# Kernel optimization log

Measured on AMD Instinct MI355X. Metric: run time of the kernel, lower is better.

The kernel has to match this reference:

```python
import jax, jax.numpy as jnp
import numpy as np

H = 51  # hidden size hard-coded in the module

def _lstm_cell(x_t, h, c, W_ih, W_hh, b_ih, b_hh):
    # PyTorch LSTMCell gate order: i, f, g, o
    gates = x_t @ W_ih.T + b_ih + h @ W_hh.T + b_hh  # [B, 4H]
    i, f, g, o = jnp.split(gates, 4, axis=-1)
    c_new = jax.nn.sigmoid(f) * c + jax.nn.sigmoid(i) * jnp.tanh(g)
    h_new = jax.nn.sigmoid(o) * jnp.tanh(c_new)
    return h_new, c_new


def setup_inputs() -> dict:
    key = jax.random.key(0)
    ks = jax.random.split(key, 11)
    B, T = 4096, 1024
    s = 1.0 / np.sqrt(H)
    return {
        "x": jax.random.normal(ks[0], (B, T), jnp.float32),
        "W_ih1": jax.random.uniform(ks[1], (4 * H, 1), jnp.float32, -s, s),
        "W_hh1": jax.random.uniform(ks[2], (4 * H, H), jnp.float32, -s, s),
        "b_ih1": jax.random.uniform(ks[3], (4 * H,), jnp.float32, -s, s),
        "b_hh1": jax.random.uniform(ks[4], (4 * H,), jnp.float32, -s, s),
        "W_ih2": jax.random.uniform(ks[5], (4 * H, H), jnp.float32, -s, s),
        "W_hh2": jax.random.uniform(ks[6], (4 * H, H), jnp.float32, -s, s),
        "b_ih2": jax.random.uniform(ks[7], (4 * H,), jnp.float32, -s, s),
        "b_hh2": jax.random.uniform(ks[8], (4 * H,), jnp.float32, -s, s),
        "W_lin": jax.random.uniform(ks[9], (1, H), jnp.float32, -s, s),
        "b_lin": jax.random.uniform(ks[10], (1,), jnp.float32, -s, s),
        "future": 64,
    }


def reference(x, W_ih1, W_hh1, b_ih1, b_hh1, W_ih2, W_hh2, b_ih2, b_hh2, W_lin, b_lin, future):
    B = x.shape[0]
    zeros = jnp.zeros((B, H), x.dtype)

    def step(carry, x_t):
        h1, c1, h2, c2 = carry
        h1, c1 = _lstm_cell(x_t, h1, c1, W_ih1, W_hh1, b_ih1, b_hh1)
        h2, c2 = _lstm_cell(h1, h2, c2, W_ih2, W_hh2, b_ih2, b_hh2)
        out = h2 @ W_lin.T + b_lin  # [B, 1]
        return (h1, c1, h2, c2), out

    xs = x.T[:, :, None]  # [T, B, 1]
    carry, outs = jax.lax.scan(step, (zeros, zeros, zeros, zeros), xs)

    def fut_step(carry, _):
        (h1, c1, h2, c2), out = carry
        h1, c1 = _lstm_cell(out, h1, c1, W_ih1, W_hh1, b_ih1, b_hh1)
        h2, c2 = _lstm_cell(h1, h2, c2, W_ih2, W_hh2, b_ih2, b_hh2)
        out = h2 @ W_lin.T + b_lin
        return ((h1, c1, h2, c2), out), out

    if future > 0:
        last_out = outs[-1]
        _, fut_outs = jax.lax.scan(fut_step, (carry, last_out), None, length=future)
        outs = jnp.concatenate([outs, fut_outs], axis=0)  # [T+future, B, 1]

    return outs[:, :, 0].T  # [B, T+future]
```

## Files before the change

kernel.cpp:

```cpp
#include <hip/hip_runtime.h>

#define HH    51
#define T_SEQ 1024
#define T_TOT 1088
#define B_TOT 4096
#define MT    16
#define NTH   512

typedef __attribute__((ext_vector_type(8))) short bf8_t;
typedef __attribute__((ext_vector_type(4))) float f32x4;

#define H1H_O 0
#define H1L_O 4096
#define H2H_O 8192
#define H2L_O 12288
#define XB_O  16384
#define OB_O  18432
#define PT_O  20480
#define SM_SZ 20992

#define L2E 1.44269504088896f

#if __has_builtin(__builtin_amdgcn_exp2f)
#define FEXP2 __builtin_amdgcn_exp2f
#else
#define FEXP2 exp2f
#endif
#if __has_builtin(__builtin_amdgcn_rcpf)
#define FRCP __builtin_amdgcn_rcpf
#else
#define FRCP(v) (1.f / (v))
#endif

__device__ __forceinline__ short f2bf(float f) {
  unsigned u = __builtin_bit_cast(unsigned, f);
  u += 0x7fffu + ((u >> 16) & 1u);
  return (short)(u >> 16);
}
__device__ __forceinline__ float bf2f(short s) {
  unsigned u = ((unsigned)(unsigned short)s) << 16;
  return __builtin_bit_cast(float, u);
}

__device__ __forceinline__ f32x4 MFMA(bf8_t a, bf8_t b, f32x4 c) {
  return __builtin_amdgcn_mfma_f32_16x16x32_bf16(a, b, c, 0, 0, 0);
}
__device__ __forceinline__ bf8_t ldA(const char* base, int row, int off) {
  off ^= ((row & 7) << 4);
  return *reinterpret_cast<const bf8_t*>(base + row * 128 + off);
}
__device__ __forceinline__ void sthl(char* WH, char* WL, int row, int boff, float v) {
  const int o = row * 128 + (boff ^ ((row & 7) << 4));
  const unsigned u = __builtin_bit_cast(unsigned, v);
  *reinterpret_cast<short*>(WH + o) = (short)(u >> 16);
  const float rem = v - __builtin_bit_cast(float, u & 0xffff0000u);
  *reinterpret_cast<short*>(WL + o) = (short)(__builtin_bit_cast(unsigned, rem) >> 16);
}

__global__ __launch_bounds__(NTH, 1)
void lstm_mfma_kernel(const float* __restrict__ x,
                      const float* __restrict__ Wih1, const float* __restrict__ Whh1,
                      const float* __restrict__ bih1, const float* __restrict__ bhh1,
                      const float* __restrict__ Wih2, const float* __restrict__ Whh2,
                      const float* __restrict__ bih2, const float* __restrict__ bhh2,
                      const float* __restrict__ Wlin, const float* __restrict__ blin,
                      float* __restrict__ out)
{
  extern __shared__ char smc[];
  float* smf = (float*)smc;
  const int tid  = threadIdx.x;
  const int lane = tid & 63;
  const int w    = tid >> 6;
  const int cl   = lane & 15;
  const int gr   = lane >> 4;
  const int rng  = w & 3;
  const bool isL2 = (w >= 4);
  const int jo   = rng * 16 + cl;
  const bool jv  = (jo < HH);
  const int bg0  = blockIdx.x * MT;

  for (int i = tid; i < SM_SZ / 4; i += NTH) smf[i] = 0.f;

  const float gsc[4] = {-L2E, -L2E, 2.f * L2E, -L2E};

  bf8_t Bh[4][4], Bl[4][4];
  #pragma unroll
  for (int g = 0; g < 4; ++g) {
    #pragma unroll
    for (int kb = 0; kb < 4; ++kb) {
      bf8_t vh, vl;
      const bool dead = (!isL2 && kb >= 2);
      const float* Wsrc = isL2 ? (kb < 2 ? Wih2 : Whh2) : Whh1;
      const int kbase = (kb & 1) * 32;
      #pragma unroll
      for (int s = 0; s < 8; ++s) {
        const int ku = kbase + gr * 8 + s;
        float v = (!dead && jv && ku < HH) ? Wsrc[(g * HH + jo) * HH + ku] * gsc[g] : 0.f;
        if (!isL2 && kb == 1 && ku == 53) v = jv ? Wih1[g * HH + jo] * gsc[g] : 0.f;
        const short hh = f2bf(v);
        vh[s] = hh;
        vl[s] = f2bf(v - bf2f(hh));
      }
      Bh[g][kb] = vh; Bl[g][kb] = vl;
    }
  }
  bf8_t Bo[2];
  #pragma unroll
  for (int kb = 0; kb < 2; ++kb) {
    bf8_t v;
    #pragma unroll
    for (int s = 0; s < 8; ++s) {
      const int ku = kb * 32 + gr * 8 + s;
      float wv = (ku < HH) ? Wlin[ku] : 0.f;
      const short hh = f2bf(wv);
      v[s] = (cl == 0) ? hh : (cl == 1) ? f2bf(wv - bf2f(hh)) : (short)0;
    }
    Bo[kb] = v;
  }
  float cbv[4], wih1v[4];
  #pragma unroll
  for (int g = 0; g < 4; ++g) {
    cbv[g]   = jv ? (isL2 ? (bih2[g*HH+jo] + bhh2[g*HH+jo])
                          : (bih1[g*HH+jo] + bhh1[g*HH+jo])) * gsc[g] : 0.f;
    wih1v[g] = (jv && !isL2) ? Wih1[g*HH+jo] * gsc[g] : 0.f;
  }
  const float wlv = (jv && isL2) ? Wlin[jo] : 0.f;
  const float bl  = blin[0];
  float cst[4] = {0.f, 0.f, 0.f, 0.f};

  auto act_h = [&](const f32x4 acc[4], int r) -> float {
    const float a0 = 1.f + FEXP2(acc[0][r]);
    const float a1 = 1.f + FEXP2(acc[1][r]);
    const float a2 = 1.f + FEXP2(acc[2][r]);
    const float a3 = 1.f + FEXP2(acc[3][r]);
    const float P02 = FRCP(a0 * a2);
    const float P13 = FRCP(a1 * a3);
    const float sitg = (a2 - 2.f) * P02;
    const float sf = a3 * P13;
    const float so = a1 * P13;
    const float cn = sf * cst[r] + sitg;
    cst[r] = cn;
    const float a4 = 1.f + FEXP2(cn * (2.f * L2E));
    return so * (1.f - 2.f * FRCP(a4));
  };

  auto writeOB = [&](int tw, const float ov[4]) {
    if (cl == 0) {
      const int po = (tw >> 4) & 1, cc = tw & 15;
      #pragma unroll
      for (int r = 0; r < 4; ++r)
        smf[OB_O/4 + po*256 + (gr*4 + r)*16 + cc] = ov[r];
    }
  };

  auto do_l1 = [&](const int p, const float* xv, const int t) {
    const char* RH = smc + H1H_O + (p ^ 1) * 2048;
    const char* RL = smc + H1L_O + (p ^ 1) * 2048;
    bf8_t a0 = ldA(RH, cl, gr*16), a1 = ldA(RH, cl, 64 + gr*16);
    bf8_t l0 = ldA(RL, cl, gr*16), l1 = ldA(RL, cl, 64 + gr*16);
    f32x4 acc[4];
    __builtin_amdgcn_s_setprio(1);
    #pragma unroll
    for (int g = 0; g < 4; ++g) {
      f32x4 a = {cbv[g], cbv[g], cbv[g], cbv[g]};
      a = MFMA(a0, Bh[g][0], a); a = MFMA(a1, Bh[g][1], a);
      a = MFMA(l0, Bh[g][0], a); a = MFMA(l1, Bh[g][1], a);
      a = MFMA(a0, Bl[g][0], a); a = MFMA(a1, Bl[g][1], a);
      acc[g] = a;
    }
    __builtin_amdgcn_s_setprio(0);
    if (xv) {
      #pragma unroll
      for (int g = 0; g < 4; ++g)
        #pragma unroll
        for (int r = 0; r < 4; ++r) acc[g][r] += wih1v[g] * xv[r];
    }
    char* WH = smc + H1H_O + p * 2048;
    char* WL = smc + H1L_O + p * 2048;
    #pragma unroll
    for (int r = 0; r < 4; ++r) {
      const float hv = act_h(acc, r);
      if (jv) sthl(WH, WL, gr * 4 + r, 2 * jo, hv);
    }
    if (!xv && rng == 3 && (t + 1) < T_SEQ) {
      if (lane < 16) {
        const float xn = smf[XB_O/4 + (((t+1) >> 4) & 1) * 256 + lane * 16 + ((t+1) & 15)];
        sthl(WH, WL, lane, 2 * 53, xn);
      }
    }
  };

  auto do_l2 = [&](const int q, const bool ar, const int tw) {
    const char* R1H = smc + H1H_O + q * 2048,       *R1L = smc + H1L_O + q * 2048;
    const char* R2H = smc + H2H_O + (q ^ 1) * 2048, *R2L = smc + H2L_O + (q ^ 1) * 2048;
    bf8_t a[4], al[4];
    a[0]  = ldA(R1H, cl, gr*16); a[1]  = ldA(R1H, cl, 64 + gr*16);
    a[2]  = ldA(R2H, cl, gr*16); a[3]  = ldA(R2H, cl, 64 + gr*16);
    al[0] = ldA(R1L, cl, gr*16); al[1] = ldA(R1L, cl, 64 + gr*16);
    al[2] = ldA(R2L, cl, gr*16); al[3] = ldA(R2L, cl, 64 + gr*16);
    f32x4 acc[4];
    f32x4 d = {0.f, 0.f, 0.f, 0.f};
    __builtin_amdgcn_s_setprio(1);
    #pragma unroll
    for (int g = 0; g < 4; ++g) {
      f32x4 ac = {cbv[g], cbv[g], cbv[g], cbv[g]};
      #pragma unroll
      for (int kb = 0; kb < 4; ++kb) ac = MFMA(a[kb],  Bh[g][kb], ac);
      #pragma unroll
      for (int kb = 0; kb < 4; ++kb) ac = MFMA(al[kb], Bh[g][kb], ac);
      #pragma unroll
      for (int kb = 0; kb < 4; ++kb) ac = MFMA(a[kb],  Bl[g][kb], ac);
      acc[g] = ac;
    }
    if (!ar && rng == 0) {
      d = MFMA(a[3], Bo[1], d); d = MFMA(a[2], Bo[0], d);
      d = MFMA(al[3], Bo[1], d); d = MFMA(al[2], Bo[0], d);
    }
    __builtin_amdgcn_s_setprio(0);
    char* WH = smc + H2H_O + q * 2048;
    char* WL = smc + H2L_O + q * 2048;
    float po[4];
    #pragma unroll
    for (int r = 0; r < 4; ++r) {
      const float hv = act_h(acc, r);
      if (jv) sthl(WH, WL, gr * 4 + r, 2 * jo, hv);
      po[r] = wlv * hv;
    }
    if (!ar) {
      if (rng == 0 && tw >= 0) {
        float ov[4];
        #pragma unroll
        for (int r = 0; r < 4; ++r) ov[r] = d[r] + __shfl_xor(d[r], 1, 64) + bl;
        writeOB(tw, ov);
      }
    } else {
      #pragma unroll
      for (int r = 0; r < 4; ++r) {
        #pragma unroll
        for (int m = 1; m < 16; m <<= 1) po[r] += __shfl_xor(po[r], m, 64);
      }
      if (cl == 0) {
        #pragma unroll
        for (int r = 0; r < 4; ++r)
          smf[PT_O/4 + q*64 + rng*16 + gr*4 + r] = po[r];
      }
    }
  };

  auto finalize = [&](const int q, float ov[4]) {
    #pragma unroll
    for (int r = 0; r < 4; ++r) {
      const int row = gr * 4 + r;
      ov[r] = smf[PT_O/4 + q*64 +  0 + row] + smf[PT_O/4 + q*64 + 16 + row]
            + smf[PT_O/4 + q*64 + 32 + row] + smf[PT_O/4 + q*64 + 48 + row] + bl;
    }
  };
  auto flushOB = [&](int tb) {
    const int q = (tb >> 4) & 1;
    #pragma unroll
    for (int it = 0; it < 4; ++it) {
      const int idx = lane + 64 * it;
      const int r = idx >> 4, tt = idx & 15;
      out[(size_t)(bg0 + r) * T_TOT + tb + tt] = smf[OB_O/4 + q*256 + r*16 + tt];
    }
  };

  __syncthreads();
  if (tid < 256) {
    const int r = tid >> 4, tt = tid & 15;
    smf[XB_O/4 + r*16 + tt] = x[(size_t)(bg0 + r) * T_SEQ + tt];
  }
  if (tid < 16)
    sthl(smc + H1H_O + 2048, smc + H1L_O + 2048, tid, 2 * 53,
         x[(size_t)(bg0 + tid) * T_SEQ]);
  __syncthreads();

  auto main_step = [&](int t, const int p) {
    if (!isL2) {
      if ((w == 1 || w == 2) && (t & 15) == 0 && (t + 16) < T_SEQ) {
        const int nt = t + 16, par = (nt >> 4) & 1;
        #pragma unroll
        for (int it = 0; it < 2; ++it) {
          const int idx = (w - 1) * 128 + lane + 64 * it;
          const int r = idx >> 4, tt = idx & 15;
          smf[XB_O/4 + par*256 + r*16 + tt] = x[(size_t)(bg0 + r) * T_SEQ + nt + tt];
        }
      }
      if (w == 3 && (t & 15) == 9 && t >= 25) flushOB(((t - 2) & ~15) - 16);
      do_l1(p, nullptr, t);
    } else {
      if (t >= 1) do_l2(p ^ 1, false, t - 2);
    }
  };

  #pragma unroll 1
  for (int t = 0; t < T_SEQ; t += 2) {
    main_step(t, 0);
    __syncthreads();
    main_step(t + 1, 1);
    __syncthreads();
  }
  if (isL2) {
    do_l2(1, true, -1);
    if (rng == 0) {
      const char* RH = smc + H2H_O;
      const char* RL = smc + H2L_O;
      bf8_t a2 = ldA(RH, cl, gr*16), a3 = ldA(RH, cl, 64 + gr*16);
      bf8_t b2 = ldA(RL, cl, gr*16), b3 = ldA(RL, cl, 64 + gr*16);
      f32x4 d = {0.f, 0.f, 0.f, 0.f};
      d = MFMA(a3, Bo[1], d); d = MFMA(a2, Bo[0], d);
      d = MFMA(b3, Bo[1], d); d = MFMA(b2, Bo[0], d);
      float ov[4];
      #pragma unroll
      for (int r = 0; r < 4; ++r) ov[r] = d[r] + __shfl_xor(d[r], 1, 64) + bl;
      writeOB(1022, ov);
    }
  } else if (w == 3 && lane < 16) {
    sthl(smc + H1H_O,        smc + H1L_O,        lane, 2 * 53, 0.f);
    sthl(smc + H1H_O + 2048, smc + H1L_O + 2048, lane, 2 * 53, 0.f);
  }
  __syncthreads();

  auto ar_step = [&](int t, const int p) {
    if (!isL2) {
      float ov[4];
      finalize(p ^ 1, ov);
      if (w == 0) writeOB(t - 1, ov);
      if (w == 3 && (t & 15) == 8) flushOB(((t - 1) & ~15) - 16);
      do_l1(p, ov, t);
    }
    __syncthreads();
    if (isL2) do_l2(p, true, -1);
    __syncthreads();
  };
  #pragma unroll 1
  for (int t = T_SEQ; t < T_TOT; t += 2) {
    ar_step(t, 0);
    ar_step(t + 1, 1);
  }
  if (!isL2 && w == 0) { float ov[4]; finalize(1, ov); writeOB(T_TOT - 1, ov); }
  __syncthreads();
  if (w == 3) flushOB(T_TOT - 16);
}

extern "C" void kernel_launch(void* const* d_in, const int* in_sizes, int n_in,
                              void* d_out, int out_size, void* d_ws, size_t ws_size,
                              hipStream_t stream) {
  const float* x    = (const float*)d_in[0];
  const float* Wih1 = (const float*)d_in[1];
  const float* Whh1 = (const float*)d_in[2];
  const float* bih1 = (const float*)d_in[3];
  const float* bhh1 = (const float*)d_in[4];
  const float* Wih2 = (const float*)d_in[5];
  const float* Whh2 = (const float*)d_in[6];
  const float* bih2 = (const float*)d_in[7];
  const float* bhh2 = (const float*)d_in[8];
  const float* Wlin = (const float*)d_in[9];
  const float* blin = (const float*)d_in[10];
  float* out = (float*)d_out;

  lstm_mfma_kernel<<<B_TOT / MT, NTH, SM_SZ, stream>>>(
      x, Wih1, Whh1, bih1, bhh1, Wih2, Whh2, bih2, bhh2, Wlin, blin, out);
}
```

Measured before the change: 1.300 ms.

## Move output projection to layer-1 warp and split layer-2 MFMA by input

Layer 2 now does its MFMAs in two phases: first over the layer-1 hidden state, then, after a scheduling barrier, over its own recurrent state. This spreads the LDS loads out and lowers register pressure. The linear output projection moves from an L2 warp onto warp 0 of the L1 group, which reads the previous layer-2 state and writes the output buffer, shortening the L2 critical path. Priority boosting changes from per-MFMA-block setprio to a whole-kernel raised priority for the L2 warps. The risk is extra work on the L1 side, and the timing of the h2 read relative to the barriers must stay correct.

```diff
diff --git a/kernel.cpp b/kernel.cpp
--- a/kernel.cpp
+++ b/kernel.cpp
@@ -159,7 +159,6 @@
     bf8_t a0 = ldA(RH, cl, gr*16), a1 = ldA(RH, cl, 64 + gr*16);
     bf8_t l0 = ldA(RL, cl, gr*16), l1 = ldA(RL, cl, 64 + gr*16);
     f32x4 acc[4];
-    __builtin_amdgcn_s_setprio(1);
     #pragma unroll
     for (int g = 0; g < 4; ++g) {
       f32x4 a = {cbv[g], cbv[g], cbv[g], cbv[g]};
@@ -168,7 +167,6 @@
       a = MFMA(a0, Bl[g][0], a); a = MFMA(a1, Bl[g][1], a);
       acc[g] = a;
     }
-    __builtin_amdgcn_s_setprio(0);
     if (xv) {
       #pragma unroll
       for (int g = 0; g < 4; ++g)
@@ -190,33 +188,31 @@
     }
   };
 
-  auto do_l2 = [&](const int q, const bool ar, const int tw) {
-    const char* R1H = smc + H1H_O + q * 2048,       *R1L = smc + H1L_O + q * 2048;
-    const char* R2H = smc + H2H_O + (q ^ 1) * 2048, *R2L = smc + H2L_O + (q ^ 1) * 2048;
-    bf8_t a[4], al[4];
-    a[0]  = ldA(R1H, cl, gr*16); a[1]  = ldA(R1H, cl, 64 + gr*16);
-    a[2]  = ldA(R2H, cl, gr*16); a[3]  = ldA(R2H, cl, 64 + gr*16);
-    al[0] = ldA(R1L, cl, gr*16); al[1] = ldA(R1L, cl, 64 + gr*16);
-    al[2] = ldA(R2L, cl, gr*16); al[3] = ldA(R2L, cl, 64 + gr*16);
+  auto do_l2 = [&](const int q, const bool ar) {
+    const char* R1H = smc + H1H_O + q * 2048, *R1L = smc + H1L_O + q * 2048;
+    bf8_t a0 = ldA(R1H, cl, gr*16), a1 = ldA(R1H, cl, 64 + gr*16);
+    bf8_t u0 = ldA(R1L, cl, gr*16), u1 = ldA(R1L, cl, 64 + gr*16);
     f32x4 acc[4];
-    f32x4 d = {0.f, 0.f, 0.f, 0.f};
-    __builtin_amdgcn_s_setprio(1);
     #pragma unroll
     for (int g = 0; g < 4; ++g) {
       f32x4 ac = {cbv[g], cbv[g], cbv[g], cbv[g]};
-      #pragma unroll
-      for (int kb = 0; kb < 4; ++kb) ac = MFMA(a[kb],  Bh[g][kb], ac);
-      #pragma unroll
-      for (int kb = 0; kb < 4; ++kb) ac = MFMA(al[kb], Bh[g][kb], ac);
-      #pragma unroll
-      for (int kb = 0; kb < 4; ++kb) ac = MFMA(a[kb],  Bl[g][kb], ac);
+      ac = MFMA(a0, Bh[g][0], ac); ac = MFMA(a1, Bh[g][1], ac);
+      ac = MFMA(u0, Bh[g][0], ac); ac = MFMA(u1, Bh[g][1], ac);
+      ac = MFMA(a0, Bl[g][0], ac); ac = MFMA(a1, Bl[g][1], ac);
       acc[g] = ac;
     }
-    if (!ar && rng == 0) {
-      d = MFMA(a[3], Bo[1], d); d = MFMA(a[2], Bo[0], d);
-      d = MFMA(al[3], Bo[1], d); d = MFMA(al[2], Bo[0], d);
-    }
-    __builtin_amdgcn_s_setprio(0);
+    __builtin_amdgcn_sched_barrier(0);
+    const char* R2H = smc + H2H_O + (q ^ 1) * 2048, *R2L = smc + H2L_O + (q ^ 1) * 2048;
+    bf8_t b0 = ldA(R2H, cl, gr*16), b1 = ldA(R2H, cl, 64 + gr*16);
+    bf8_t v0 = ldA(R2L, cl, gr*16), v1 = ldA(R2L, cl, 64 + gr*16);
+    #pragma unroll
+    for (int g = 0; g < 4; ++g) {
+      f32x4 ac = acc[g];
+      ac = MFMA(b0, Bh[g][2], ac); ac = MFMA(b1, Bh[g][3], ac);
+      ac = MFMA(v0, Bh[g][2], ac); ac = MFMA(v1, Bh[g][3], ac);
+      ac = MFMA(b0, Bl[g][2], ac); ac = MFMA(b1, Bl[g][3], ac);
+      acc[g] = ac;
+    }
     char* WH = smc + H2H_O + q * 2048;
     char* WL = smc + H2L_O + q * 2048;
     float po[4];
@@ -226,14 +222,7 @@
       if (jv) sthl(WH, WL, gr * 4 + r, 2 * jo, hv);
       po[r] = wlv * hv;
     }
-    if (!ar) {
-      if (rng == 0 && tw >= 0) {
-        float ov[4];
-        #pragma unroll
-        for (int r = 0; r < 4; ++r) ov[r] = d[r] + __shfl_xor(d[r], 1, 64) + bl;
-        writeOB(tw, ov);
-      }
-    } else {
+    if (ar) {
       #pragma unroll
       for (int r = 0; r < 4; ++r) {
         #pragma unroll
@@ -274,6 +263,8 @@
     sthl(smc + H1H_O + 2048, smc + H1L_O + 2048, tid, 2 * 53,
          x[(size_t)(bg0 + tid) * T_SEQ]);
   __syncthreads();
+
+  if (isL2) __builtin_amdgcn_s_setprio(1);
 
   auto main_step = [&](int t, const int p) {
     if (!isL2) {
@@ -288,8 +279,21 @@
       }
       if (w == 3 && (t & 15) == 9 && t >= 25) flushOB(((t - 2) & ~15) - 16);
       do_l1(p, nullptr, t);
+      if (w == 0 && t >= 2) {
+        const char* PH = smc + H2H_O + p * 2048;
+        const char* PL = smc + H2L_O + p * 2048;
+        bf8_t b0 = ldA(PH, cl, gr*16), b1 = ldA(PH, cl, 64 + gr*16);
+        bf8_t v0 = ldA(PL, cl, gr*16), v1 = ldA(PL, cl, 64 + gr*16);
+        f32x4 d = {0.f, 0.f, 0.f, 0.f};
+        d = MFMA(b1, Bo[1], d); d = MFMA(b0, Bo[0], d);
+        d = MFMA(v1, Bo[1], d); d = MFMA(v0, Bo[0], d);
+        float ov[4];
+        #pragma unroll
+        for (int r = 0; r < 4; ++r) ov[r] = d[r] + __shfl_xor(d[r], 1, 64) + bl;
+        writeOB(t - 2, ov);
+      }
     } else {
-      if (t >= 1) do_l2(p ^ 1, false, t - 2);
+      if (t >= 1) do_l2(p ^ 1, false);
     }
   };
 
@@ -301,7 +305,7 @@
     __syncthreads();
   }
   if (isL2) {
-    do_l2(1, true, -1);
+    do_l2(1, true);
     if (rng == 0) {
       const char* RH = smc + H2H_O;
       const char* RL = smc + H2L_O;
@@ -330,7 +334,7 @@
       do_l1(p, ov, t);
     }
     __syncthreads();
-    if (isL2) do_l2(p, true, -1);
+    if (isL2) do_l2(p, true);
     __syncthreads();
   };
   #pragma unroll 1
```

New measurement: 1.218 ms (median of 2 runs). -6.4%, faster.
